# Kernel tuning notes

Measured on AMD Instinct MI355X. Metric: run time of the kernel, lower is better.

The kernel has to match this reference:

```python
import jax, jax.numpy as jnp
import numpy as np

IN_F = 4096
OUT_F = 4096
GROUP = 8
N_GROUPS = OUT_F * IN_F // GROUP  # 2097152
BATCH = 32


def _dequant_3bit(weight_q3, weight_norm):
    # weight_q3: [G, 3] bytes (stored int32, values 0..255)
    # weight_norm: [G, 1] fp16 per-group abs-max scale
    p = weight_q3.astype(jnp.int32)
    val = p[:, 0] | (p[:, 1] << 8) | (p[:, 2] << 16)          # [G] 24-bit word
    shifts = jnp.arange(GROUP, dtype=jnp.int32) * 3           # [8]
    q = ((val[:, None] >> shifts[None, :]) & 7).astype(jnp.float32)  # [G, 8] in {0..7}
    n = weight_norm.astype(jnp.float32)                        # [G, 1]
    w = (q / 7.0) * (2.0 * n) - n                              # de-normalize to [-n, n]
    return w.reshape(OUT_F, IN_F)


def setup_inputs() -> dict:
    key = jax.random.key(0)
    k1, k2, k3, k4 = jax.random.split(key, 4)
    x = jax.random.normal(k1, (BATCH, IN_F), dtype=jnp.float32)
    weight_q3 = jax.random.randint(k2, (N_GROUPS, 3), 0, 256, dtype=jnp.int32)
    weight_norm = jax.random.uniform(k3, (N_GROUPS, 1), dtype=jnp.float16, minval=0.01, maxval=1.0)
    bias = jax.random.normal(k4, (OUT_F,), dtype=jnp.float32)
    return {"x": x, "weight_q3": weight_q3, "weight_norm": weight_norm, "bias": bias}


def reference(x, weight_q3, weight_norm, bias):
    w = _dequant_3bit(weight_q3, weight_norm)  # [OUT_F, IN_F] fp32
    return x @ w.T + bias                      # F.linear semantics
```

## Files before the change

kernel.cpp:

```cpp
#include <hip/hip_runtime.h>
#include <hip/hip_fp16.h>

#define IN_F   4096
#define OUT_F  4096
#define BATCH  32
#define NGPR   512
#define BN     16
#define NW     4
#define QP     260
#define NP     260

typedef float f32x4  __attribute__((ext_vector_type(4)));
typedef short short8 __attribute__((ext_vector_type(8)));

__device__ __forceinline__ unsigned short f2bf_u(float f) {
    return __builtin_bit_cast(unsigned short, (__bf16)f);
}

__global__ __launch_bounds__(256)
void pack_x_kernel(const float* __restrict__ x, unsigned short* __restrict__ apk)
{
    const int tau = blockIdx.x * 256 + threadIdx.x;
    const int row = tau >> 9;
    const int c   = tau & 511;
    const float4 lo = *reinterpret_cast<const float4*>(&x[row * IN_F + c * 8]);
    const float4 hi = *reinterpret_cast<const float4*>(&x[row * IN_F + c * 8 + 4]);
    union { unsigned short us[8]; uint4 v; } pk;
    pk.us[0] = f2bf_u(lo.x); pk.us[1] = f2bf_u(lo.y);
    pk.us[2] = f2bf_u(lo.z); pk.us[3] = f2bf_u(lo.w);
    pk.us[4] = f2bf_u(hi.x); pk.us[5] = f2bf_u(hi.y);
    pk.us[6] = f2bf_u(hi.z); pk.us[7] = f2bf_u(hi.w);
    const int a = row >> 4, cl = row & 15, s = c >> 2, q = c & 3;
    const int unit = (a * 128 + s) * 64 + q * 16 + cl;
    *reinterpret_cast<uint4*>(&apk[unit * 8]) = pk.v;
}

template<bool PACKED>
__global__ __launch_bounds__(256, 3)
void l3b_main(const float* __restrict__ x,
              const int* __restrict__ wq3,
              const void* __restrict__ wnorm_raw,
              const float* __restrict__ bias,
              float* __restrict__ out,
              const unsigned short* __restrict__ apk)
{
    __shared__ unsigned int qw[BN][QP];
    __shared__ float        nrm[BN][NP];
    __shared__ float        red[NW][BATCH][17];

    const int tid   = threadIdx.x;
    const int w     = tid >> 6;
    const int lane  = tid & 63;
    const int nbase = (blockIdx.x >> 1) * BN;
    const int kh    = blockIdx.x & 1;

    const int q  = lane >> 4;
    const int cl = lane & 15;

    const unsigned short* wn16  = (const unsigned short*)wnorm_raw;
    const float*          wn32  = (const float*)wnorm_raw;
    const unsigned int*   wnu32 = (const unsigned int*)wnorm_raw;
    int mode;
    {
        const unsigned short h = wn16[lane];
        const float v16 = __half2float(__builtin_bit_cast(__half, h));
        const float vbf = __builtin_bit_cast(float, (unsigned int)h << 16);
        const float v32 = wn32[lane];
        const int c16 = __popcll(__ballot(v16 > 0.0095f && v16 < 1.0005f));
        const int cbf = __popcll(__ballot(vbf > 0.0095f && vbf < 1.0005f));
        const int c32 = __popcll(__ballot(v32 > 0.0095f && v32 < 1.0005f));
        if (c16 >= c32 && c16 >= cbf) {
            mode = 1;
        } else if (c32 > cbf + 8) {
            mode = 0;
        } else if (cbf > c32 + 8) {
            mode = 2;
        } else {
            const int z = __popcll(__ballot((wnu32[lane] & 0x1FFFu) == 0u));
            mode = (z >= 48) ? 0 : 2;
        }
    }

    if (mode == 0) {
        const float* nb = wn32 + (long)nbase * NGPR + kh * 256;
        #pragma unroll
        for (int j = 0; j < 4; ++j) {
            const int e = j * 1024 + tid * 4;
            const int row = e >> 8, col = e & 255;
            const float4 v = *reinterpret_cast<const float4*>(nb + (long)row * NGPR + col);
            *reinterpret_cast<float4*>(&nrm[row][col]) = v;
        }
    } else {
        const unsigned short* nb = wn16 + (long)nbase * NGPR + kh * 256;
        #pragma unroll
        for (int j = 0; j < 2; ++j) {
            const int e = j * 2048 + tid * 8;
            const int row = e >> 8, col = e & 255;
            union { unsigned short us[8]; uint4 v; } u;
            u.v = *reinterpret_cast<const uint4*>(nb + (long)row * NGPR + col);
            float4 f0, f1;
            if (mode == 1) {
                f0.x = __half2float(__builtin_bit_cast(__half, u.us[0]));
                f0.y = __half2float(__builtin_bit_cast(__half, u.us[1]));
                f0.z = __half2float(__builtin_bit_cast(__half, u.us[2]));
                f0.w = __half2float(__builtin_bit_cast(__half, u.us[3]));
                f1.x = __half2float(__builtin_bit_cast(__half, u.us[4]));
                f1.y = __half2float(__builtin_bit_cast(__half, u.us[5]));
                f1.z = __half2float(__builtin_bit_cast(__half, u.us[6]));
                f1.w = __half2float(__builtin_bit_cast(__half, u.us[7]));
            } else {
                f0.x = __builtin_bit_cast(float, (unsigned)u.us[0] << 16);
                f0.y = __builtin_bit_cast(float, (unsigned)u.us[1] << 16);
                f0.z = __builtin_bit_cast(float, (unsigned)u.us[2] << 16);
                f0.w = __builtin_bit_cast(float, (unsigned)u.us[3] << 16);
                f1.x = __builtin_bit_cast(float, (unsigned)u.us[4] << 16);
                f1.y = __builtin_bit_cast(float, (unsigned)u.us[5] << 16);
                f1.z = __builtin_bit_cast(float, (unsigned)u.us[6] << 16);
                f1.w = __builtin_bit_cast(float, (unsigned)u.us[7] << 16);
            }
            *reinterpret_cast<float4*>(&nrm[row][col])     = f0;
            *reinterpret_cast<float4*>(&nrm[row][col + 4]) = f1;
        }
    }

    {
        const int* qgbase = wq3 + (long)nbase * 1536 + kh * 768;
        #pragma unroll
        for (int r2 = 0; r2 < 4; ++r2) {
            const int row = r2 * 4 + (tid >> 6);
            const int cb  = (tid & 63) * 12;
            const int* p = qgbase + (long)row * 1536 + cb;
            const int4 ia = *reinterpret_cast<const int4*>(p);
            const int4 ib = *reinterpret_cast<const int4*>(p + 4);
            const int4 ic = *reinterpret_cast<const int4*>(p + 8);
            uint4 wd;
            wd.x = (unsigned)(ia.x | (ia.y << 8) | (ia.z << 16));
            wd.y = (unsigned)(ia.w | (ib.x << 8) | (ib.y << 16));
            wd.z = (unsigned)(ib.z | (ib.w << 8) | (ic.x << 16));
            wd.w = (unsigned)(ic.y | (ic.z << 8) | (ic.w << 16));
            *reinterpret_cast<uint4*>(&qw[row][(tid & 63) * 4]) = wd;
        }
    }

    __syncthreads();

    f32x4 acc0 = {0.f, 0.f, 0.f, 0.f};
    f32x4 acc1 = {0.f, 0.f, 0.f, 0.f};

    #pragma unroll 4
    for (int i = 0; i < 16; ++i) {
        const int s = w * 16 + i;
        const int g = s * 4 + q;

        const unsigned int qv = qw[cl][g];
        const float n  = nrm[cl][g];
        const float av = n * 0.285714285714285714f;
        union { unsigned short us[8]; short8 v; } B;
        #pragma unroll
        for (int e = 0; e < 8; ++e) {
            const float qf = (float)((qv >> (3 * e)) & 7u);
            B.us[e] = f2bf_u(fmaf(qf, av, -n));
        }

        const int sg = kh * 64 + s;
        short8 A0, A1;
        if (PACKED) {
            A0 = *reinterpret_cast<const short8*>(&apk[(sg * 64 + lane) * 8]);
            A1 = *reinterpret_cast<const short8*>(&apk[((128 + sg) * 64 + lane) * 8]);
        } else {
            const int kg = sg * 32 + q * 8;
            const float4 a0lo = *reinterpret_cast<const float4*>(&x[cl        * IN_F + kg]);
            const float4 a0hi = *reinterpret_cast<const float4*>(&x[cl        * IN_F + kg + 4]);
            const float4 a1lo = *reinterpret_cast<const float4*>(&x[(cl + 16) * IN_F + kg]);
            const float4 a1hi = *reinterpret_cast<const float4*>(&x[(cl + 16) * IN_F + kg + 4]);
            union { unsigned short us[8]; short8 v; } U0, U1;
            U0.us[0] = f2bf_u(a0lo.x); U0.us[1] = f2bf_u(a0lo.y);
            U0.us[2] = f2bf_u(a0lo.z); U0.us[3] = f2bf_u(a0lo.w);
            U0.us[4] = f2bf_u(a0hi.x); U0.us[5] = f2bf_u(a0hi.y);
            U0.us[6] = f2bf_u(a0hi.z); U0.us[7] = f2bf_u(a0hi.w);
            U1.us[0] = f2bf_u(a1lo.x); U1.us[1] = f2bf_u(a1lo.y);
            U1.us[2] = f2bf_u(a1lo.z); U1.us[3] = f2bf_u(a1lo.w);
            U1.us[4] = f2bf_u(a1hi.x); U1.us[5] = f2bf_u(a1hi.y);
            U1.us[6] = f2bf_u(a1hi.z); U1.us[7] = f2bf_u(a1hi.w);
            A0 = U0.v; A1 = U1.v;
        }

        acc0 = __builtin_amdgcn_mfma_f32_16x16x32_bf16(A0, B.v, acc0, 0, 0, 0);
        acc1 = __builtin_amdgcn_mfma_f32_16x16x32_bf16(A1, B.v, acc1, 0, 0, 0);
    }

    #pragma unroll
    for (int i = 0; i < 4; ++i) {
        red[w][q * 4 + i][cl]      = acc0[i];
        red[w][16 + q * 4 + i][cl] = acc1[i];
    }
    __syncthreads();
    {
        const int m  = tid >> 4;
        const int nl = tid & 15;
        float s1 = 0.f, s2 = 0.f;
        #pragma unroll
        for (int wv = 0; wv < NW; ++wv) {
            s1 += red[wv][m][nl];
            s2 += red[wv][m + 16][nl];
        }
        const float b = (kh == 0) ? bias[nbase + nl] : 0.0f;
        atomicAdd(&out[m * OUT_F + nbase + nl], s1 + b);
        atomicAdd(&out[(m + 16) * OUT_F + nbase + nl], s2 + b);
    }
}

extern "C" void kernel_launch(void* const* d_in, const int* in_sizes, int n_in,
                              void* d_out, int out_size, void* d_ws, size_t ws_size,
                              hipStream_t stream) {
    const float* x    = (const float*)d_in[0];
    const int*   wq3  = (const int*)d_in[1];
    const void*  wn   = (const void*)d_in[2];
    const float* bias = (const float*)d_in[3];
    float*       out  = (float*)d_out;

    hipMemsetAsync(d_out, 0, (size_t)BATCH * OUT_F * sizeof(float), stream);

    if (ws_size >= (size_t)(2 * 128 * 64 * 8 * 2)) {
        unsigned short* apk = (unsigned short*)d_ws;
        pack_x_kernel<<<dim3(64), dim3(256), 0, stream>>>(x, apk);
        l3b_main<true><<<dim3(512), dim3(256), 0, stream>>>(x, wq3, wn, bias, out, apk);
    } else {
        l3b_main<false><<<dim3(512), dim3(256), 0, stream>>>(x, wq3, wn, bias, out, nullptr);
    }
}
```

Before: 19.80 us.

## Drop split-K atomics and stage raw int32 weights into LDS via direct loads

Each block now covers the full K range for 16 outputs, using 512 threads and eight waves instead of two split-K blocks of 256 threads. The result is written directly with bias, so the output memset and the atomic adds go away. The raw int32 weight bytes are copied global-to-LDS with global_load_lds instead of being repacked through registers, and the three bytes are combined when read from LDS. In exchange, LDS use per block rises to about 148KB and the grid halves to 256 blocks, which may limit occupancy and latency hiding.

```diff
diff --git a/kernel.cpp b/kernel.cpp
--- a/kernel.cpp
+++ b/kernel.cpp
@@ -6,15 +6,21 @@
 #define BATCH  32
 #define NGPR   512
 #define BN     16
-#define NW     4
-#define QP     260
-#define NP     260
+#define NW     8
+#define QPITCH 1540
+#define NPITCH 516
 
 typedef float f32x4  __attribute__((ext_vector_type(4)));
 typedef short short8 __attribute__((ext_vector_type(8)));
 
 __device__ __forceinline__ unsigned short f2bf_u(float f) {
     return __builtin_bit_cast(unsigned short, (__bf16)f);
+}
+
+__device__ __forceinline__ void gload16(const void* gsrc, void* lds) {
+    __builtin_amdgcn_global_load_lds(
+        (const __attribute__((address_space(1))) void*)gsrc,
+        (__attribute__((address_space(3))) void*)lds, 16, 0, 0);
 }
 
 __global__ __launch_bounds__(256)
@@ -36,7 +42,7 @@
 }
 
 template<bool PACKED>
-__global__ __launch_bounds__(256, 3)
+__global__ __launch_bounds__(512, 2)
 void l3b_main(const float* __restrict__ x,
               const int* __restrict__ wq3,
               const void* __restrict__ wnorm_raw,
@@ -44,15 +50,14 @@
               float* __restrict__ out,
               const unsigned short* __restrict__ apk)
 {
-    __shared__ unsigned int qw[BN][QP];
-    __shared__ float        nrm[BN][NP];
+    __shared__ unsigned int qls[BN * QPITCH];
+    __shared__ float        nrm[BN][NPITCH];
     __shared__ float        red[NW][BATCH][17];
 
     const int tid   = threadIdx.x;
     const int w     = tid >> 6;
     const int lane  = tid & 63;
-    const int nbase = (blockIdx.x >> 1) * BN;
-    const int kh    = blockIdx.x & 1;
+    const int nbase = blockIdx.x * BN;
 
     const int q  = lane >> 4;
     const int cl = lane & 15;
@@ -81,23 +86,34 @@
         }
     }
 
+    {
+        const int* qg = wq3 + (long)nbase * 1536;
+        #pragma unroll
+        for (int rr = 0; rr < 2; ++rr) {
+            const int row = w * 2 + rr;
+            #pragma unroll
+            for (int i = 0; i < 6; ++i) {
+                const int off = i * 256 + lane * 4;
+                gload16(qg + (long)row * 1536 + off, &qls[row * QPITCH + off]);
+            }
+        }
+    }
+
     if (mode == 0) {
-        const float* nb = wn32 + (long)nbase * NGPR + kh * 256;
+        const float* nb = wn32 + (long)nbase * NGPR;
         #pragma unroll
         for (int j = 0; j < 4; ++j) {
-            const int e = j * 1024 + tid * 4;
-            const int row = e >> 8, col = e & 255;
-            const float4 v = *reinterpret_cast<const float4*>(nb + (long)row * NGPR + col);
-            *reinterpret_cast<float4*>(&nrm[row][col]) = v;
+            const int f = j * 2048 + tid * 4;
+            const float4 v = *reinterpret_cast<const float4*>(nb + f);
+            *reinterpret_cast<float4*>(&nrm[f >> 9][f & 511]) = v;
         }
     } else {
-        const unsigned short* nb = wn16 + (long)nbase * NGPR + kh * 256;
+        const unsigned short* nb = wn16 + (long)nbase * NGPR;
         #pragma unroll
         for (int j = 0; j < 2; ++j) {
-            const int e = j * 2048 + tid * 8;
-            const int row = e >> 8, col = e & 255;
+            const int f = j * 4096 + tid * 8;
             union { unsigned short us[8]; uint4 v; } u;
-            u.v = *reinterpret_cast<const uint4*>(nb + (long)row * NGPR + col);
+            u.v = *reinterpret_cast<const uint4*>(nb + f);
             float4 f0, f1;
             if (mode == 1) {
                 f0.x = __half2float(__builtin_bit_cast(__half, u.us[0]));
@@ -118,27 +134,9 @@
                 f1.z = __builtin_bit_cast(float, (unsigned)u.us[6] << 16);
                 f1.w = __builtin_bit_cast(float, (unsigned)u.us[7] << 16);
             }
+            const int row = f >> 9, col = f & 511;
             *reinterpret_cast<float4*>(&nrm[row][col])     = f0;
             *reinterpret_cast<float4*>(&nrm[row][col + 4]) = f1;
-        }
-    }
-
-    {
-        const int* qgbase = wq3 + (long)nbase * 1536 + kh * 768;
-        #pragma unroll
-        for (int r2 = 0; r2 < 4; ++r2) {
-            const int row = r2 * 4 + (tid >> 6);
-            const int cb  = (tid & 63) * 12;
-            const int* p = qgbase + (long)row * 1536 + cb;
-            const int4 ia = *reinterpret_cast<const int4*>(p);
-            const int4 ib = *reinterpret_cast<const int4*>(p + 4);
-            const int4 ic = *reinterpret_cast<const int4*>(p + 8);
-            uint4 wd;
-            wd.x = (unsigned)(ia.x | (ia.y << 8) | (ia.z << 16));
-            wd.y = (unsigned)(ia.w | (ib.x << 8) | (ib.y << 16));
-            wd.z = (unsigned)(ib.z | (ib.w << 8) | (ic.x << 16));
-            wd.w = (unsigned)(ic.y | (ic.z << 8) | (ic.w << 16));
-            *reinterpret_cast<uint4*>(&qw[row][(tid & 63) * 4]) = wd;
         }
     }
 
@@ -152,23 +150,27 @@
         const int s = w * 16 + i;
         const int g = s * 4 + q;
 
-        const unsigned int qv = qw[cl][g];
+        const int qb = cl * QPITCH + g * 3;
+        const unsigned d0 = qls[qb];
+        const unsigned d1 = qls[qb + 1];
+        const unsigned d2 = qls[qb + 2];
+        const unsigned val = (d0 & 0xFFu) | ((d1 & 0xFFu) << 8) | ((d2 & 0xFFu) << 16);
+
         const float n  = nrm[cl][g];
         const float av = n * 0.285714285714285714f;
         union { unsigned short us[8]; short8 v; } B;
         #pragma unroll
         for (int e = 0; e < 8; ++e) {
-            const float qf = (float)((qv >> (3 * e)) & 7u);
+            const float qf = (float)((val >> (3 * e)) & 7u);
             B.us[e] = f2bf_u(fmaf(qf, av, -n));
         }
 
-        const int sg = kh * 64 + s;
         short8 A0, A1;
         if (PACKED) {
-            A0 = *reinterpret_cast<const short8*>(&apk[(sg * 64 + lane) * 8]);
-            A1 = *reinterpret_cast<const short8*>(&apk[((128 + sg) * 64 + lane) * 8]);
+            A0 = *reinterpret_cast<const short8*>(&apk[(s * 64 + lane) * 8]);
+            A1 = *reinterpret_cast<const short8*>(&apk[((128 + s) * 64 + lane) * 8]);
         } else {
-            const int kg = sg * 32 + q * 8;
+            const int kg = s * 32 + q * 8;
             const float4 a0lo = *reinterpret_cast<const float4*>(&x[cl        * IN_F + kg]);
             const float4 a0hi = *reinterpret_cast<const float4*>(&x[cl        * IN_F + kg + 4]);
             const float4 a1lo = *reinterpret_cast<const float4*>(&x[(cl + 16) * IN_F + kg]);
@@ -198,15 +200,10 @@
     {
         const int m  = tid >> 4;
         const int nl = tid & 15;
-        float s1 = 0.f, s2 = 0.f;
-        #pragma unroll
-        for (int wv = 0; wv < NW; ++wv) {
-            s1 += red[wv][m][nl];
-            s2 += red[wv][m + 16][nl];
-        }
-        const float b = (kh == 0) ? bias[nbase + nl] : 0.0f;
-        atomicAdd(&out[m * OUT_F + nbase + nl], s1 + b);
-        atomicAdd(&out[(m + 16) * OUT_F + nbase + nl], s2 + b);
+        float ssum = 0.f;
+        #pragma unroll
+        for (int wv = 0; wv < NW; ++wv) ssum += red[wv][m][nl];
+        out[m * OUT_F + nbase + nl] = ssum + bias[nbase + nl];
     }
 }
 
@@ -219,13 +216,11 @@
     const float* bias = (const float*)d_in[3];
     float*       out  = (float*)d_out;
 
-    hipMemsetAsync(d_out, 0, (size_t)BATCH * OUT_F * sizeof(float), stream);
-
     if (ws_size >= (size_t)(2 * 128 * 64 * 8 * 2)) {
         unsigned short* apk = (unsigned short*)d_ws;
         pack_x_kernel<<<dim3(64), dim3(256), 0, stream>>>(x, apk);
-        l3b_main<true><<<dim3(512), dim3(256), 0, stream>>>(x, wq3, wn, bias, out, apk);
+        l3b_main<true><<<dim3(OUT_F / BN), dim3(512), 0, stream>>>(x, wq3, wn, bias, out, apk);
     } else {
-        l3b_main<false><<<dim3(512), dim3(256), 0, stream>>>(x, wq3, wn, bias, out, nullptr);
-    }
-}
+        l3b_main<false><<<dim3(OUT_F / BN), dim3(512), 0, stream>>>(x, wq3, wn, bias, out, nullptr);
+    }
+}
```

Result: faster. 17.22 us (-13.0%).
